# Kernel tuning notes

Hardware: AMD Instinct MI355X
Metric: run time of the kernel (lower is better)

Reference implementation:

```python
import jax, jax.numpy as jnp
import numpy as np

TOTAL_INSTANCES = 131072
NUM_BAGS = 64
FEATURE_DIM = 512
HIDDEN_DIM = 256


def setup_inputs() -> dict:
    key = jax.random.key(0)
    k1, k2, k3 = jax.random.split(key, 3)
    instance_features = jax.random.normal(k1, (TOTAL_INSTANCES, FEATURE_DIM), dtype=jnp.float32)
    # Equal-sized bags (sum(bag_sizes) == TOTAL_INSTANCES); the reference handles ragged sizes too.
    bag_sizes = jnp.full((NUM_BAGS,), TOTAL_INSTANCES // NUM_BAGS, dtype=jnp.int32)
    W1 = jax.random.normal(k2, (FEATURE_DIM, HIDDEN_DIM), dtype=jnp.float32) * (1.0 / np.sqrt(FEATURE_DIM))
    b1 = jnp.zeros((HIDDEN_DIM,), dtype=jnp.float32)
    W2 = jax.random.normal(k3, (HIDDEN_DIM, 1), dtype=jnp.float32) * (1.0 / np.sqrt(HIDDEN_DIM))
    b2 = jnp.zeros((1,), dtype=jnp.float32)
    return {
        "instance_features": instance_features,
        "bag_sizes": bag_sizes,
        "W1": W1,
        "b1": b1,
        "W2": W2,
        "b2": b2,
    }


def reference(instance_features, bag_sizes, W1, b1, W2, b2):
    # Attention MLP: Linear -> Tanh -> Linear  => scores [T, 1]
    scores = jnp.tanh(instance_features @ W1 + b1) @ W2 + b2
    # Faithful to the original: softmax over dim=0 GLOBALLY across all instances.
    weights = jax.nn.softmax(scores, axis=0)  # [T, 1]
    T = instance_features.shape[0]
    B = bag_sizes.shape[0]
    # Ragged bag membership: instance i belongs to the first bag whose cumulative
    # size exceeds i.
    offsets = jnp.cumsum(bag_sizes)  # [B]
    seg_ids = jnp.searchsorted(offsets, jnp.arange(T), side="right")  # [T]
    # Per-bag weighted sum of instances: [B, feature_dim]
    return jax.ops.segment_sum(instance_features * weights, seg_ids, num_segments=B)
```

## Files before the change

### kernel.cpp

```cpp
#include <hip/hip_runtime.h>

typedef __attribute__((ext_vector_type(8))) short short8;
typedef __attribute__((ext_vector_type(4))) float floatx4;

#define FDIM 512
#define HDIM 256

__device__ __forceinline__ unsigned short f2bf(float f) {
  unsigned int u = __float_as_uint(f);
  u += 0x7fffu + ((u >> 16) & 1u);
  return (unsigned short)(u >> 16);
}

__device__ __forceinline__ short8 pack2(floatx4 a, floatx4 b) {
  short8 r;
  r[0] = (short)f2bf(a[0]); r[1] = (short)f2bf(a[1]);
  r[2] = (short)f2bf(a[2]); r[3] = (short)f2bf(a[3]);
  r[4] = (short)f2bf(b[0]); r[5] = (short)f2bf(b[1]);
  r[6] = (short)f2bf(b[2]); r[7] = (short)f2bf(b[3]);
  return r;
}

__device__ __forceinline__ float fast_tanh(float x) {
  x = fminf(15.0f, fmaxf(-15.0f, x));
  float e = __expf(2.0f * x);
  return (e - 1.0f) / (e + 1.0f);
}

__device__ __forceinline__ void gload_lds16(const void* g, void* l) {
  __builtin_amdgcn_global_load_lds(
      (const __attribute__((address_space(1))) unsigned int*)g,
      (__attribute__((address_space(3))) unsigned int*)l, 16, 0, 0);
}

#define GLOAD_SET(r0, r1, p)                                                   \
  do {                                                                         \
    asm volatile("global_load_dwordx4 %0, %1, off"                             \
                 : "=v"(r0) : "v"(p) : "memory");                              \
    asm volatile("global_load_dwordx4 %0, %1, off offset:16"                   \
                 : "=v"(r1) : "v"(p) : "memory");                              \
  } while (0)

__global__ void __launch_bounds__(256)
k0_pack_w1(const float* __restrict__ W1, unsigned short* __restrict__ W1B,
           float* __restrict__ out) {
  int tid = threadIdx.x;
  int idx = blockIdx.x * 256 + tid;
  if (blockIdx.x < 128) out[blockIdx.x * 256 + tid] = 0.0f;
  int k = idx >> 8;
  int n = idx & 255;
  int s = k >> 5, r = k & 31, oct = r >> 3, e = r & 7;
  W1B[s * 8192 + oct * 2048 + n * 8 + e] = f2bf(W1[idx]);
}

__global__ void __launch_bounds__(512)
k1_fused(const float* __restrict__ X,
         const unsigned short* __restrict__ W1B,
         const float* __restrict__ b1,
         const float* __restrict__ W2,
         const int* __restrict__ bag_sizes,
         int nbags,
         float* __restrict__ out,
         float* __restrict__ partials) {
  __shared__ __align__(16) unsigned char smem[163840];
  unsigned short* As  = (unsigned short*)smem;
  unsigned short* Bs0 = (unsigned short*)(smem + 131072);
  unsigned short* Bs1 = (unsigned short*)(smem + 147456);
  float* scpart = (float*)(smem + 131072);
  float* es_s   = (float*)(smem + 131072 + 2048);
  float* wsum_s = (float*)(smem + 131072 + 2560);

  const int tid  = threadIdx.x;
  const int wid  = tid >> 6;
  const int lane = tid & 63;
  const int l15  = lane & 15;
  const int l4   = lane >> 4;
  const int wr   = wid >> 2;
  const int wn   = wid & 3;
  const long row0 = (long)blockIdx.x * 128;

  floatx4 acc[4][4];
  #pragma unroll
  for (int m = 0; m < 4; m++)
    #pragma unroll
    for (int n = 0; n < 4; n++)
      acc[m][n] = (floatx4){0.f, 0.f, 0.f, 0.f};

  const int arow = tid >> 2;
  const int aoct = tid & 3;
  const float* xsrc = X + (row0 + arow) * FDIM + aoct * 8;

  floatx4 va0, va1, vb0, vb1;

  GLOAD_SET(va0, va1, xsrc);
  #pragma unroll
  for (int i = 0; i < 2; ++i)
    gload_lds16(W1B + (i * 512 + tid) * 8, Bs0 + (i * 512 + wid * 64) * 8);
  GLOAD_SET(vb0, vb1, xsrc + 32);

  #pragma unroll
  for (int t = 0; t < 16; ++t) {
    unsigned short* Bcur = (t & 1) ? Bs1 : Bs0;
    if (t < 15) asm volatile("s_waitcnt vmcnt(4)" ::: "memory");
    else        asm volatile("s_waitcnt vmcnt(2)" ::: "memory");
    __builtin_amdgcn_sched_barrier(0);
    {
      short8 a = ((t & 1) == 0) ? pack2(va0, va1) : pack2(vb0, vb1);
      int slot = t * 4 + aoct;
      *(short8*)(As + (slot * 128 + (arow ^ (slot & 7))) * 8) = a;
    }
    asm volatile("s_waitcnt lgkmcnt(0)" ::: "memory");
    if (t < 15) asm volatile("s_waitcnt vmcnt(2)" ::: "memory");
    else        asm volatile("s_waitcnt vmcnt(0)" ::: "memory");
    __builtin_amdgcn_sched_barrier(0);
    __builtin_amdgcn_s_barrier();
    if (t < 15) {
      unsigned short* Bn = (t & 1) ? Bs0 : Bs1;
      #pragma unroll
      for (int i = 0; i < 2; ++i)
        gload_lds16(W1B + (t + 1) * 8192 + (i * 512 + tid) * 8,
                    Bn + (i * 512 + wid * 64) * 8);
    }
    if (t < 14) {
      const float* pp = xsrc + (t + 2) * 32;
      if ((t & 1) == 0) GLOAD_SET(va0, va1, pp);
      else              GLOAD_SET(vb0, vb1, pp);
    }
    const int slotc = t * 4 + l4;
    const int gg = slotc & 7;
    short8 af[4];
    #pragma unroll
    for (int m = 0; m < 4; ++m)
      af[m] = *(const short8*)(As + (slotc * 128 + ((wr * 64 + m * 16 + l15) ^ gg)) * 8);
    #pragma unroll
    for (int n = 0; n < 4; ++n) {
      short8 bfr = *(const short8*)(Bcur + (l4 * 256 + wn * 64 + n * 16 + l15) * 8);
      #pragma unroll
      for (int m = 0; m < 4; ++m)
        acc[m][n] = __builtin_amdgcn_mfma_f32_16x16x32_bf16(af[m], bfr, acc[m][n], 0, 0, 0);
    }
  }

  float rowacc[16];
  #pragma unroll
  for (int i = 0; i < 16; i++) rowacc[i] = 0.f;
  #pragma unroll
  for (int n = 0; n < 4; n++) {
    int c = wn * 64 + n * 16 + l15;
    float b1c = b1[c];
    float w2c = W2[c];
    #pragma unroll
    for (int m = 0; m < 4; m++)
      #pragma unroll
      for (int j = 0; j < 4; j++) {
        float h = fast_tanh(acc[m][n][j] + b1c);
        rowacc[m * 4 + j] = fmaf(h, w2c, rowacc[m * 4 + j]);
      }
  }
  #pragma unroll
  for (int i = 0; i < 16; i++) {
    float v = rowacc[i];
    v += __shfl_xor(v, 1, 64);
    v += __shfl_xor(v, 2, 64);
    v += __shfl_xor(v, 4, 64);
    v += __shfl_xor(v, 8, 64);
    rowacc[i] = v;
  }
  if (l15 == 0) {
    #pragma unroll
    for (int m = 0; m < 4; m++)
      #pragma unroll
      for (int j = 0; j < 4; j++)
        scpart[wn * 128 + wr * 64 + m * 16 + l4 * 4 + j] = rowacc[m * 4 + j];
  }
  __syncthreads();

  if (tid < 128) {
    float sv = scpart[0 * 128 + tid] + scpart[1 * 128 + tid] +
               scpart[2 * 128 + tid] + scpart[3 * 128 + tid];
    float ev = __expf(sv);
    es_s[tid] = ev;
    float v = ev;
    v += __shfl_xor(v, 1, 64);
    v += __shfl_xor(v, 2, 64);
    v += __shfl_xor(v, 4, 64);
    v += __shfl_xor(v, 8, 64);
    v += __shfl_xor(v, 16, 64);
    v += __shfl_xor(v, 32, 64);
    if (lane == 0) wsum_s[wid] = v;
  }
  __syncthreads();
  if (tid == 0) partials[blockIdx.x] = wsum_s[0] + wsum_s[1];

  const int s  = tid >> 3;
  const int p  = tid & 7;
  const int gp = s & 7;
  const int fbase = (s >> 2) * 32 + (s & 3) * 8;
  const unsigned short* abase = As + s * 1024;

  int bag = 0; long cum = 0;
  while (bag + 1 < nbags && cum + (long)bag_sizes[bag] <= row0) {
    cum += bag_sizes[bag]; ++bag;
  }
  long bagEnd = cum + (long)bag_sizes[bag];

  int rs = 0;
  while (rs < 128) {
    int se = (int)(bagEnd - row0 < 128 ? bagEnd - row0 : 128);
    float pa[8];
    #pragma unroll
    for (int e = 0; e < 8; ++e) pa[e] = 0.f;
    #pragma unroll
    for (int j = 0; j < 16; ++j) {
      int r = p + 8 * j;
      if (r >= rs && r < se) {
        float w = es_s[r];
        short8 xv = *(const short8*)(abase + ((r ^ gp) * 8));
        const unsigned int* ui = (const unsigned int*)&xv;
        #pragma unroll
        for (int d = 0; d < 4; ++d) {
          float xlo = __uint_as_float(ui[d] << 16);
          float xhi = __uint_as_float(ui[d] & 0xffff0000u);
          pa[2 * d]     = fmaf(xlo, w, pa[2 * d]);
          pa[2 * d + 1] = fmaf(xhi, w, pa[2 * d + 1]);
        }
      }
    }
    #pragma unroll
    for (int e = 0; e < 8; ++e) {
      pa[e] += __shfl_xor(pa[e], 1, 64);
      pa[e] += __shfl_xor(pa[e], 2, 64);
      pa[e] += __shfl_xor(pa[e], 4, 64);
    }
    if (p == 0 && se > rs) {
      float* op = out + (long)bag * FDIM + fbase;
      #pragma unroll
      for (int e = 0; e < 8; ++e) atomicAdd(op + e, pa[e]);
    }
    rs = se;
    if (rs < 128) {
      ++bag;
      if (bag >= nbags) { bagEnd = row0 + 128; bag = nbags - 1; }
      else bagEnd += (long)bag_sizes[bag];
    }
  }
}

__global__ void __launch_bounds__(256)
k2_scale(const float* __restrict__ partials, int nparts, float* __restrict__ out) {
  __shared__ float wred[4];
  int tid = threadIdx.x;
  float sL = 0.f;
  for (int j = tid; j < nparts; j += 256) sL += partials[j];
  #pragma unroll
  for (int m = 1; m < 64; m <<= 1) sL += __shfl_xor(sL, m, 64);
  if ((tid & 63) == 0) wred[tid >> 6] = sL;
  __syncthreads();
  float invZ = 1.0f / (wred[0] + wred[1] + wred[2] + wred[3]);
  int i = blockIdx.x * 256 + tid;
  out[i] = out[i] * invZ;
}

extern "C" void kernel_launch(void* const* d_in, const int* in_sizes, int n_in,
                              void* d_out, int out_size, void* d_ws, size_t ws_size,
                              hipStream_t stream) {
  const float* X         = (const float*)d_in[0];
  const int*   bag_sizes = (const int*)d_in[1];
  const float* W1        = (const float*)d_in[2];
  const float* b1        = (const float*)d_in[3];
  const float* W2        = (const float*)d_in[4];
  float* out = (float*)d_out;

  const int T     = in_sizes[0] / FDIM;
  const int nbags = in_sizes[1];
  const int nblk  = T / 128;

  char* ws = (char*)d_ws;
  unsigned short* W1B = (unsigned short*)ws;
  float* partials = (float*)(ws + 262144);

  hipLaunchKernelGGL(k0_pack_w1, dim3(512), dim3(256), 0, stream, W1, W1B, out);
  hipLaunchKernelGGL(k1_fused, dim3(nblk), dim3(512), 0, stream,
                     X, W1B, b1, W2, bag_sizes, nbags, out, partials);
  hipLaunchKernelGGL(k2_scale, dim3((nbags * FDIM) / 256), dim3(256), 0, stream,
                     partials, nblk, out);
}
```

Before: 109.4 us.

## Halve row tile, load W1 fragments directly into registers, fit two blocks per CU

The fused kernel now processes 64 rows per block with 256 threads instead of 128 rows with 512. It drops the LDS staging of W1 and has each wave load its bf16 W1 fragments straight into registers with a three-slot rotating prefetch. Shared memory falls to about 66KB, which lets two blocks share a CU and doubles the grid. In exchange, every block now re-reads W1 from global/L2, so W1 traffic grows and register pressure rises from the extra fragment buffers. The softmax partial count doubles and the bag reduction is adjusted to match.

```diff
diff --git a/kernel.cpp b/kernel.cpp
--- a/kernel.cpp
+++ b/kernel.cpp
@@ -27,18 +27,24 @@
   return (e - 1.0f) / (e + 1.0f);
 }
 
-__device__ __forceinline__ void gload_lds16(const void* g, void* l) {
-  __builtin_amdgcn_global_load_lds(
-      (const __attribute__((address_space(1))) unsigned int*)g,
-      (__attribute__((address_space(3))) unsigned int*)l, 16, 0, 0);
-}
-
-#define GLOAD_SET(r0, r1, p)                                                   \
+#define GLOAD_A(r0, r1, p)                                                     \
   do {                                                                         \
     asm volatile("global_load_dwordx4 %0, %1, off"                             \
                  : "=v"(r0) : "v"(p) : "memory");                              \
     asm volatile("global_load_dwordx4 %0, %1, off offset:16"                   \
                  : "=v"(r1) : "v"(p) : "memory");                              \
+  } while (0)
+
+#define GLOAD_B(r, p)                                                          \
+  do {                                                                         \
+    asm volatile("global_load_dwordx4 %0, %1, off"                             \
+                 : "=v"(r[0]) : "v"(p) : "memory");                            \
+    asm volatile("global_load_dwordx4 %0, %1, off offset:256"                  \
+                 : "=v"(r[1]) : "v"(p) : "memory");                            \
+    asm volatile("global_load_dwordx4 %0, %1, off offset:512"                  \
+                 : "=v"(r[2]) : "v"(p) : "memory");                            \
+    asm volatile("global_load_dwordx4 %0, %1, off offset:768"                  \
+                 : "=v"(r[3]) : "v"(p) : "memory");                            \
   } while (0)
 
 __global__ void __launch_bounds__(256)
@@ -53,7 +59,7 @@
   W1B[s * 8192 + oct * 2048 + n * 8 + e] = f2bf(W1[idx]);
 }
 
-__global__ void __launch_bounds__(512)
+__global__ void __launch_bounds__(256, 2)
 k1_fused(const float* __restrict__ X,
          const unsigned short* __restrict__ W1B,
          const float* __restrict__ b1,
@@ -62,22 +68,17 @@
          int nbags,
          float* __restrict__ out,
          float* __restrict__ partials) {
-  __shared__ __align__(16) unsigned char smem[163840];
-  unsigned short* As  = (unsigned short*)smem;
-  unsigned short* Bs0 = (unsigned short*)(smem + 131072);
-  unsigned short* Bs1 = (unsigned short*)(smem + 147456);
-  float* scpart = (float*)(smem + 131072);
-  float* es_s   = (float*)(smem + 131072 + 2048);
-  float* wsum_s = (float*)(smem + 131072 + 2560);
+  __shared__ __align__(16) unsigned char smem[66816];
+  unsigned short* As = (unsigned short*)smem;
+  float* scpart = (float*)(smem + 65536);
+  float* es_s   = (float*)(smem + 66560);
 
   const int tid  = threadIdx.x;
-  const int wid  = tid >> 6;
+  const int wn   = tid >> 6;
   const int lane = tid & 63;
   const int l15  = lane & 15;
   const int l4   = lane >> 4;
-  const int wr   = wid >> 2;
-  const int wn   = wid & 3;
-  const long row0 = (long)blockIdx.x * 128;
+  const long row0 = (long)blockIdx.x * 64;
 
   floatx4 acc[4][4];
   #pragma unroll
@@ -89,56 +90,54 @@
   const int arow = tid >> 2;
   const int aoct = tid & 3;
   const float* xsrc = X + (row0 + arow) * FDIM + aoct * 8;
+  const unsigned short* bsrc = W1B + l4 * 2048 + (wn * 64 + l15) * 8;
 
   floatx4 va0, va1, vb0, vb1;
-
-  GLOAD_SET(va0, va1, xsrc);
-  #pragma unroll
-  for (int i = 0; i < 2; ++i)
-    gload_lds16(W1B + (i * 512 + tid) * 8, Bs0 + (i * 512 + wid * 64) * 8);
-  GLOAD_SET(vb0, vb1, xsrc + 32);
+  short8 br0[4], br1[4], br2[4];
+
+  GLOAD_A(va0, va1, xsrc);
+  GLOAD_B(br0, bsrc);
+  GLOAD_A(vb0, vb1, xsrc + 32);
+  GLOAD_B(br1, bsrc + 8192);
 
   #pragma unroll
   for (int t = 0; t < 16; ++t) {
-    unsigned short* Bcur = (t & 1) ? Bs1 : Bs0;
-    if (t < 15) asm volatile("s_waitcnt vmcnt(4)" ::: "memory");
-    else        asm volatile("s_waitcnt vmcnt(2)" ::: "memory");
+    if (t < 15) asm volatile("s_waitcnt vmcnt(10)" ::: "memory");
+    else        asm volatile("s_waitcnt vmcnt(4)" ::: "memory");
     __builtin_amdgcn_sched_barrier(0);
     {
       short8 a = ((t & 1) == 0) ? pack2(va0, va1) : pack2(vb0, vb1);
       int slot = t * 4 + aoct;
-      *(short8*)(As + (slot * 128 + (arow ^ (slot & 7))) * 8) = a;
+      *(short8*)(As + (slot * 64 + (arow ^ (slot & 7))) * 8) = a;
     }
     asm volatile("s_waitcnt lgkmcnt(0)" ::: "memory");
-    if (t < 15) asm volatile("s_waitcnt vmcnt(2)" ::: "memory");
-    else        asm volatile("s_waitcnt vmcnt(0)" ::: "memory");
     __builtin_amdgcn_sched_barrier(0);
     __builtin_amdgcn_s_barrier();
-    if (t < 15) {
-      unsigned short* Bn = (t & 1) ? Bs0 : Bs1;
-      #pragma unroll
-      for (int i = 0; i < 2; ++i)
-        gload_lds16(W1B + (t + 1) * 8192 + (i * 512 + tid) * 8,
-                    Bn + (i * 512 + wid * 64) * 8);
-    }
     if (t < 14) {
       const float* pp = xsrc + (t + 2) * 32;
-      if ((t & 1) == 0) GLOAD_SET(va0, va1, pp);
-      else              GLOAD_SET(vb0, vb1, pp);
-    }
+      if ((t & 1) == 0) GLOAD_A(va0, va1, pp);
+      else              GLOAD_A(vb0, vb1, pp);
+      const unsigned short* bp = bsrc + (t + 2) * 8192;
+      if (((t + 2) % 3) == 0)      GLOAD_B(br0, bp);
+      else if (((t + 2) % 3) == 1) GLOAD_B(br1, bp);
+      else                         GLOAD_B(br2, bp);
+    }
+    if (t < 14)       asm volatile("s_waitcnt vmcnt(12)" ::: "memory");
+    else if (t == 14) asm volatile("s_waitcnt vmcnt(6)" ::: "memory");
+    else              asm volatile("s_waitcnt vmcnt(0)" ::: "memory");
+    __builtin_amdgcn_sched_barrier(0);
     const int slotc = t * 4 + l4;
     const int gg = slotc & 7;
     short8 af[4];
     #pragma unroll
     for (int m = 0; m < 4; ++m)
-      af[m] = *(const short8*)(As + (slotc * 128 + ((wr * 64 + m * 16 + l15) ^ gg)) * 8);
-    #pragma unroll
-    for (int n = 0; n < 4; ++n) {
-      short8 bfr = *(const short8*)(Bcur + (l4 * 256 + wn * 64 + n * 16 + l15) * 8);
+      af[m] = *(const short8*)(As + (slotc * 64 + ((m * 16 + l15) ^ gg)) * 8);
+    const short8* bcur = ((t % 3) == 0) ? br0 : ((t % 3) == 1) ? br1 : br2;
+    #pragma unroll
+    for (int n = 0; n < 4; ++n)
       #pragma unroll
       for (int m = 0; m < 4; ++m)
-        acc[m][n] = __builtin_amdgcn_mfma_f32_16x16x32_bf16(af[m], bfr, acc[m][n], 0, 0, 0);
-    }
+        acc[m][n] = __builtin_amdgcn_mfma_f32_16x16x32_bf16(af[m], bcur[n], acc[m][n], 0, 0, 0);
   }
 
   float rowacc[16];
@@ -171,13 +170,13 @@
     for (int m = 0; m < 4; m++)
       #pragma unroll
       for (int j = 0; j < 4; j++)
-        scpart[wn * 128 + wr * 64 + m * 16 + l4 * 4 + j] = rowacc[m * 4 + j];
+        scpart[wn * 64 + m * 16 + l4 * 4 + j] = rowacc[m * 4 + j];
   }
   __syncthreads();
 
-  if (tid < 128) {
-    float sv = scpart[0 * 128 + tid] + scpart[1 * 128 + tid] +
-               scpart[2 * 128 + tid] + scpart[3 * 128 + tid];
+  if (tid < 64) {
+    float sv = scpart[0 * 64 + tid] + scpart[1 * 64 + tid] +
+               scpart[2 * 64 + tid] + scpart[3 * 64 + tid];
     float ev = __expf(sv);
     es_s[tid] = ev;
     float v = ev;
@@ -187,16 +186,15 @@
     v += __shfl_xor(v, 8, 64);
     v += __shfl_xor(v, 16, 64);
     v += __shfl_xor(v, 32, 64);
-    if (lane == 0) wsum_s[wid] = v;
+    if (tid == 0) partials[blockIdx.x] = v;
   }
   __syncthreads();
-  if (tid == 0) partials[blockIdx.x] = wsum_s[0] + wsum_s[1];
-
-  const int s  = tid >> 3;
-  const int p  = tid & 7;
+
+  const int s  = tid >> 2;
+  const int p  = tid & 3;
   const int gp = s & 7;
   const int fbase = (s >> 2) * 32 + (s & 3) * 8;
-  const unsigned short* abase = As + s * 1024;
+  const unsigned short* abase = As + s * 512;
 
   int bag = 0; long cum = 0;
   while (bag + 1 < nbags && cum + (long)bag_sizes[bag] <= row0) {
@@ -205,14 +203,14 @@
   long bagEnd = cum + (long)bag_sizes[bag];
 
   int rs = 0;
-  while (rs < 128) {
-    int se = (int)(bagEnd - row0 < 128 ? bagEnd - row0 : 128);
+  while (rs < 64) {
+    int se = (int)(bagEnd - row0 < 64 ? bagEnd - row0 : 64);
     float pa[8];
     #pragma unroll
     for (int e = 0; e < 8; ++e) pa[e] = 0.f;
     #pragma unroll
     for (int j = 0; j < 16; ++j) {
-      int r = p + 8 * j;
+      int r = p + 4 * j;
       if (r >= rs && r < se) {
         float w = es_s[r];
         short8 xv = *(const short8*)(abase + ((r ^ gp) * 8));
@@ -230,7 +228,6 @@
     for (int e = 0; e < 8; ++e) {
       pa[e] += __shfl_xor(pa[e], 1, 64);
       pa[e] += __shfl_xor(pa[e], 2, 64);
-      pa[e] += __shfl_xor(pa[e], 4, 64);
     }
     if (p == 0 && se > rs) {
       float* op = out + (long)bag * FDIM + fbase;
@@ -238,9 +235,9 @@
       for (int e = 0; e < 8; ++e) atomicAdd(op + e, pa[e]);
     }
     rs = se;
-    if (rs < 128) {
+    if (rs < 64) {
       ++bag;
-      if (bag >= nbags) { bagEnd = row0 + 128; bag = nbags - 1; }
+      if (bag >= nbags) { bagEnd = row0 + 64; bag = nbags - 1; }
       else bagEnd += (long)bag_sizes[bag];
     }
   }
@@ -273,14 +270,14 @@
 
   const int T     = in_sizes[0] / FDIM;
   const int nbags = in_sizes[1];
-  const int nblk  = T / 128;
+  const int nblk  = T / 64;
 
   char* ws = (char*)d_ws;
   unsigned short* W1B = (unsigned short*)ws;
   float* partials = (float*)(ws + 262144);
 
   hipLaunchKernelGGL(k0_pack_w1, dim3(512), dim3(256), 0, stream, W1, W1B, out);
-  hipLaunchKernelGGL(k1_fused, dim3(nblk), dim3(512), 0, stream,
+  hipLaunchKernelGGL(k1_fused, dim3(nblk), dim3(256), 0, stream,
                      X, W1B, b1, W2, bag_sizes, nbags, out, partials);
   hipLaunchKernelGGL(k2_scale, dim3((nbags * FDIM) / 256), dim3(256), 0, stream,
                      partials, nblk, out);
```

After: 124.6 us. 13.9% more time.
